# Performance work log

Hardware: AMD Instinct MI355X
Metric: run time of the kernel (lower is better)

Reference implementation:

```python
import jax, jax.numpy as jnp
import numpy as np

D_MODEL = 1024
N_HEADS = 16
SEQ_LEN = 2048
BATCH = 2
NEG = -1.0e9


def sinusoidal_embeddings(seq_len, d_k):
    # Faithful to the torch version: row 0 is all zeros; even cols get sin,
    # odd cols get cos of position/theta (theta uses the SAME index j, not j//2).
    theta = 10000.0 ** (2.0 * jnp.arange(d_k, dtype=jnp.float32) / d_k)  # [d_k]
    pos = jnp.arange(1, seq_len, dtype=jnp.float32)[:, None] / theta      # [S-1, d_k]
    even = (jnp.arange(d_k) % 2 == 0)
    body = jnp.where(even, jnp.sin(pos), jnp.cos(pos))                    # [S-1, d_k]
    return jnp.concatenate([jnp.zeros((1, d_k), dtype=pos.dtype), body], axis=0)


def setup_inputs() -> dict:
    key = jax.random.key(0)
    k_x, k_q, k_k, k_v, k_o = jax.random.split(key, 5)
    scale = 0.02
    return {
        "X": jax.random.normal(k_x, (BATCH, SEQ_LEN, D_MODEL), dtype=jnp.float32),
        "W_q": jax.random.normal(k_q, (D_MODEL, D_MODEL), dtype=jnp.float32) * scale,
        "W_k": jax.random.normal(k_k, (D_MODEL, D_MODEL), dtype=jnp.float32) * scale,
        "W_v": jax.random.normal(k_v, (D_MODEL, D_MODEL), dtype=jnp.float32) * scale,
        "W_o": jax.random.normal(k_o, (D_MODEL, D_MODEL), dtype=jnp.float32) * scale,
    }


def reference(X, W_q, W_k, W_v, W_o):
    B, S, D = X.shape
    H, d_k = N_HEADS, D // N_HEADS

    def proj(W):  # nn.Linear (no bias): y = x @ W.T, then split heads -> [B,H,S,d_k]
        return (X @ W.T).reshape(B, S, H, d_k).transpose(0, 2, 1, 3)

    Q, K, V = proj(W_q), proj(W_k), proj(W_v)

    pos = sinusoidal_embeddings(S, d_k)          # [S, d_k]
    Q = Q + pos
    K = K + pos

    mask = jnp.triu(jnp.full((S, S), NEG, dtype=X.dtype), k=1)  # [S,S]
    scores = jnp.einsum("bhqd,bhkd->bhqk", Q, K) / jnp.sqrt(jnp.float32(d_k)) + mask
    weights = jax.nn.softmax(scores, axis=-1)
    attn = jnp.einsum("bhqk,bhkd->bhqd", weights, V)            # [B,H,S,d_k]

    attn = attn.transpose(0, 2, 1, 3).reshape(B, S, D)
    return attn @ W_o.T + X
```

## Files before the change

### kernel.cpp

```cpp
#include <hip/hip_runtime.h>
#include <hip/hip_bf16.h>
#include <math.h>

#define S_LEN 2048
#define DMODEL 1024
#define NHEADS 16
#define DHEAD 64
#define NBATCH 2
#define MROWS (NBATCH * S_LEN)

typedef float f32x4 __attribute__((ext_vector_type(4)));
typedef unsigned short u16x8 __attribute__((ext_vector_type(8)));
typedef __bf16 bf16x8 __attribute__((ext_vector_type(8)));

__device__ __forceinline__ f32x4 mfma16(u16x8 a, u16x8 b, f32x4 c) {
    return __builtin_amdgcn_mfma_f32_16x16x32_bf16(
        __builtin_bit_cast(bf16x8, a), __builtin_bit_cast(bf16x8, b), c, 0, 0, 0);
}

__device__ __forceinline__ unsigned short f2bf(float f) {
    unsigned int u = __builtin_bit_cast(unsigned int, f);
    u += 0x7FFFu + ((u >> 16) & 1u);
    return (unsigned short)(u >> 16);
}

__device__ __forceinline__ unsigned int cvtpk(float lo, float hi) {
    unsigned int r;
    asm("v_cvt_pk_bf16_f32 %0, %1, %2" : "=v"(r) : "v"(lo), "v"(hi));
    return r;
}

__device__ __forceinline__ void gl16(const void* g, void* l) {
    __builtin_amdgcn_global_load_lds(
        (const __attribute__((address_space(1))) unsigned int*)g,
        (__attribute__((address_space(3))) unsigned int*)l, 16, 0, 0);
}

#define VMB(N) do { \
    asm volatile("s_waitcnt vmcnt(" #N ")" ::: "memory"); \
    __builtin_amdgcn_sched_barrier(0); \
    __builtin_amdgcn_s_barrier(); \
    __builtin_amdgcn_sched_barrier(0); } while (0)
#define PIPE_BAR_12() do { \
    asm volatile("s_waitcnt vmcnt(12)" ::: "memory"); \
    __builtin_amdgcn_sched_barrier(0); \
    __builtin_amdgcn_s_barrier(); \
    __builtin_amdgcn_sched_barrier(0); } while (0)
#define PIPE_BAR_0() do { \
    asm volatile("s_waitcnt vmcnt(0)" ::: "memory"); \
    __builtin_amdgcn_sched_barrier(0); \
    __builtin_amdgcn_s_barrier(); \
    __builtin_amdgcn_sched_barrier(0); } while (0)

__global__ __launch_bounds__(256) void cvt5(
    const float* __restrict__ X, const float* __restrict__ Wq,
    const float* __restrict__ Wk, const float* __restrict__ Wv,
    const float* __restrict__ Wo,
    unsigned short* __restrict__ Xbf, unsigned short* __restrict__ Wbf,
    float* __restrict__ pos)
{
    int b = blockIdx.x;
    if (b >= 4096) {
        int i = (b - 4096) * 256 + threadIdx.x;
        int s = i >> 6, d = i & 63;
        float theta = powf(10000.0f, (2.0f * (float)d) / 64.0f);
        float x = (float)s / theta;
        float v = (d & 1) ? cosf(x) : sinf(x);
        pos[i] = (s == 0) ? 0.0f : v;
        return;
    }
    const float* s; unsigned short* d; int t;
    if (b < 2048) { s = X; d = Xbf; t = b * 256 + threadIdx.x; }
    else {
        int z = (b - 2048) >> 9, bb = (b - 2048) & 511;
        s = (z == 0) ? Wq : (z == 1) ? Wk : (z == 2) ? Wv : Wo;
        d = Wbf + (z << 20);
        t = bb * 256 + threadIdx.x;
    }
    float4 a = *((const float4*)s + t * 2);
    float4 c = *((const float4*)s + t * 2 + 1);
    u16x8 o;
    o[0] = f2bf(a.x); o[1] = f2bf(a.y); o[2] = f2bf(a.z); o[3] = f2bf(a.w);
    o[4] = f2bf(c.x); o[5] = f2bf(c.y); o[6] = f2bf(c.z); o[7] = f2bf(c.w);
    *((u16x8*)d + t) = o;
}

__global__ __launch_bounds__(512) void gemm_qkv(
    const unsigned short* __restrict__ Xbf, const unsigned short* __restrict__ Wbf,
    const float* __restrict__ pos,
    unsigned short* __restrict__ qb, unsigned short* __restrict__ kb,
    unsigned short* __restrict__ vt)
{
    __shared__ unsigned short L[2][28672];
    const int t = threadIdx.x;
    const int lane = t & 63;
    const int w = t >> 6;
    const int wm = w >> 2, wn = w & 3;
    const int m0 = blockIdx.x * 256;
    const int nb = blockIdx.y * 192;
    const int ll = lane & 15, lg = lane >> 4;
    const int tr = t >> 3;
    const int ch = (t & 7) ^ (tr & 7);

    f32x4 acc[8][3] = {};

    const unsigned short* gA[4];
    const unsigned short* gB[3];
    #pragma unroll
    for (int i = 0; i < 4; i++)
        gA[i] = Xbf + (m0 + i * 64 + tr) * 1024 + ch * 8;
    #pragma unroll
    for (int i = 0; i < 3; i++)
        gB[i] = Wbf + (nb + i * 64 + tr) * 1024 + ch * 8;

    const int sw0 = ((0 * 4 + lg) ^ (ll & 7)) * 16;
    const int sw1 = ((1 * 4 + lg) ^ (ll & 7)) * 16;
    const int aBase = (wm * 128 + ll) * 128;
    const int bBase = 32768 + (wn * 48 + ll) * 128;
    const int wdst = w * 8 * 64;

    auto stB01 = [&](unsigned short* Ln) {
        gl16(gB[0], Ln + 16384 + wdst);          gB[0] += 64;
        gl16(gB[1], Ln + 16384 + 4096 + wdst);   gB[1] += 64;
    };
    auto stB2 = [&](unsigned short* Ln) {
        gl16(gB[2], Ln + 16384 + 8192 + wdst);   gB[2] += 64;
    };
    auto stA02 = [&](unsigned short* Ln) {
        gl16(gA[0], Ln + wdst);                  gA[0] += 64;
        gl16(gA[2], Ln + 8192 + wdst);           gA[2] += 64;
    };
    auto stA13 = [&](unsigned short* Ln) {
        gl16(gA[1], Ln + 4096 + wdst);           gA[1] += 64;
        gl16(gA[3], Ln + 12288 + wdst);          gA[3] += 64;
    };

    u16x8 bf[3][2];
    auto loadB = [&](const char* bB) {
        #pragma unroll
        for (int nf = 0; nf < 3; nf++) {
            const char* p = bB + bBase + nf * 2048;
            bf[nf][0] = *(const u16x8*)(p + sw0);
            bf[nf][1] = *(const u16x8*)(p + sw1);
        }
    };
    auto quad = [&](int q, const char* bA) {
        const char* pa = bA + aBase + q * 4096;
        u16x8 a00 = *(const u16x8*)(pa + sw0);
        u16x8 a01 = *(const u16x8*)(pa + sw1);
        u16x8 a10 = *(const u16x8*)(pa + 2048 + sw0);
        u16x8 a11 = *(const u16x8*)(pa + 2048 + sw1);
        __builtin_amdgcn_s_setprio(1);
        #pragma unroll
        for (int nf = 0; nf < 3; nf++) {
            acc[q * 2 + 0][nf] = mfma16(a00, bf[nf][0], acc[q * 2 + 0][nf]);
            acc[q * 2 + 1][nf] = mfma16(a10, bf[nf][0], acc[q * 2 + 1][nf]);
        }
        #pragma unroll
        for (int nf = 0; nf < 3; nf++) {
            acc[q * 2 + 0][nf] = mfma16(a01, bf[nf][1], acc[q * 2 + 0][nf]);
            acc[q * 2 + 1][nf] = mfma16(a11, bf[nf][1], acc[q * 2 + 1][nf]);
        }
        __builtin_amdgcn_s_setprio(0);
    };

    stB01(L[0]); stB2(L[0]); stA02(L[0]); stA13(L[0]);
    VMB(2);

    #pragma unroll 1
    for (int tt = 0; tt < 15; tt++) {
        const char* bA = (const char*)L[tt & 1];
        unsigned short* Ln = L[(tt + 1) & 1];
        stB01(Ln);
        loadB(bA);
        quad(0, bA);
        __builtin_amdgcn_s_barrier();
        stB2(Ln);
        quad(1, bA);
        __builtin_amdgcn_s_barrier();
        stA02(Ln);
        VMB(5);
        quad(2, bA);
        __builtin_amdgcn_s_barrier();
        stA13(Ln);
        quad(3, bA);
        VMB(2);
    }
    {
        const char* bA = (const char*)L[1];
        loadB(bA);
        quad(0, bA);
        __builtin_amdgcn_s_barrier();
        quad(1, bA);
        VMB(0);
        quad(2, bA);
        quad(3, bA);
    }

    #pragma unroll
    for (int nf = 0; nf < 3; nf++) {
        const int c = nb + wn * 48 + nf * 16 + ll;
        const int zz = c >> 10;
        const int lc = c & 1023;
        const int h = lc >> 6, d = lc & 63;
        if (zz == 2) {
            #pragma unroll
            for (int mf = 0; mf < 8; mf++) {
                const int row0 = m0 + wm * 128 + mf * 16 + lg * 4;
                const int b = row0 >> 11, s0 = row0 & 2047;
                unsigned long long pk =
                    (unsigned long long)cvtpk(acc[mf][nf][0], acc[mf][nf][1]) |
                    ((unsigned long long)cvtpk(acc[mf][nf][2], acc[mf][nf][3]) << 32);
                *(unsigned long long*)&vt[(((b * NHEADS + h) * 64) + d) * S_LEN + s0] = pk;
            }
        } else {
            unsigned short* const dst = (zz == 0) ? qb : kb;
            const float pscale = (zz == 0) ? 0.1803368801111244f : 1.0f;
            #pragma unroll
            for (int mf = 0; mf < 8; mf++) {
                #pragma unroll
                for (int r = 0; r < 4; r++) {
                    const int row = m0 + wm * 128 + mf * 16 + lg * 4 + r;
                    const int b = row >> 11, s = row & 2047;
                    float v = acc[mf][nf][r] + pos[s * 64 + d];
                    v *= pscale;
                    dst[(((b * NHEADS + h) * S_LEN) + s) * 64 + d] = f2bf(v);
                }
            }
        }
    }
}

__global__ __launch_bounds__(512, 4) void attn_kernel(
    const unsigned short* __restrict__ qb,
    const unsigned short* __restrict__ kb,
    const unsigned short* __restrict__ vt,
    unsigned short* __restrict__ attnb)
{
    __shared__ unsigned short Klds[2][128 * 64];
    __shared__ unsigned short Vlds[2][64 * 128];
    __shared__ unsigned short Plds[8][16 * 64];

    const int bh = blockIdx.y;
    const int x = blockIdx.x;
    const int qt = (bh < 16) ? (15 - x) : x;

    const int lane = threadIdx.x & 63;
    const int w = threadIdx.x >> 6;
    const int lg = lane >> 4, ll = lane & 15;
    const int r8 = lane >> 3, ch = (lane & 7) ^ r8;
    const int r4 = lane >> 4, c16 = lane & 15;

    const unsigned short* Q = qb + bh * (S_LEN * 64);
    const unsigned short* K = kb + bh * (S_LEN * 64);
    const unsigned short* V = vt + bh * (64 * S_LEN);
    const int q0 = qt * 128 + w * 16;

    u16x8 qf0 = *(const u16x8*)(Q + (q0 + ll) * 64 + lg * 8);
    u16x8 qf1 = *(const u16x8*)(Q + (q0 + ll) * 64 + 32 + lg * 8);

    u16x8 ones;
    #pragma unroll
    for (int i = 0; i < 8; i++) ones[i] = 0x3F80;

    f32x4 o_acc[4] = {};
    f32x4 l_acc = {};

    const int sw0 = ((0 * 4 + lg) ^ (ll & 7)) * 16;
    const int sw1 = ((1 * 4 + lg) ^ (ll & 7)) * 16;
    const char* kb0p0 = (const char*)&Klds[0][0] + ll * 128 + sw0;
    const char* kb0p1 = (const char*)&Klds[0][0] + ll * 128 + sw1;
    const char* kb1p0 = (const char*)&Klds[1][0] + ll * 128 + sw0;
    const char* kb1p1 = (const char*)&Klds[1][0] + ll * 128 + sw1;
    const char* vb0p0 = (const char*)&Vlds[0][0] + ll * 256 + sw0;
    const char* vb0p1 = (const char*)&Vlds[0][0] + ll * 256 + sw1;
    const char* vb1p0 = (const char*)&Vlds[1][0] + ll * 256 + sw0;
    const char* vb1p1 = (const char*)&Vlds[1][0] + ll * 256 + sw1;
    const int E = (ll & 7) << 4;
    char* pwb = (char*)&Plds[w][0] + (((ll * 128) + lg * 8) ^ (E & 16));
    const int pw_o0 = 0 ^ (E & 96), pw_o1 = 32 ^ (E & 96);
    const int pw_o2 = 64 ^ (E & 96), pw_o3 = 96 ^ (E & 96);
    const char* pr0 = (const char*)&Plds[w][0] + ll * 128 + sw0;
    const char* pr1 = (const char*)&Plds[w][0] + ll * 128 + sw1;
    unsigned short* kd0 = &Klds[0][(w * 16) * 64];
    unsigned short* kd1 = &Klds[1][(w * 16) * 64];
    unsigned short* vd0 = &Vlds[0][(w * 8) * 128];
    unsigned short* vd1 = &Vlds[1][(w * 8) * 128];
    const unsigned short* gk  = K + (w * 16 + r8) * 64 + ch * 8;
    const unsigned short* gva = V + (w * 8 + r4) * S_LEN + ((c16 ^ r4) * 8);
    const unsigned short* gvb = V + (w * 8 + 4 + r4) * S_LEN + ((c16 ^ (4 + r4)) * 8);
    const int dthr = w * 16 + ll - lg * 4;

    auto stage2 = [&](unsigned short* kd, unsigned short* vd) {
        gl16(gk, kd);
        gl16(gk + 512, kd + 512);
        gl16(gva, vd);
        gl16(gvb, vd + 512);
        gk += 128 * 64;
        gva += 128;
        gvb += 128;
    };

    auto tile_body = [&](const char* kp0, const char* kp1,
                         const char* vp0, const char* vp1, bool masked, int thr) {
        f32x4 sc[4] = {};
        __builtin_amdgcn_s_setprio(1);
        #pragma unroll
        for (int f = 0; f < 4; f++) {
            const u16x8 kfa = *(const u16x8*)(kp0 + f * 2048);
            sc[f] = mfma16(kfa, qf0, sc[f]);
            const u16x8 kfb = *(const u16x8*)(kp1 + f * 2048);
            sc[f] = mfma16(kfb, qf1, sc[f]);
        }
        __builtin_amdgcn_s_setprio(0);
        if (masked) {
            #pragma unroll
            for (int f = 0; f < 4; f++)
                #pragma unroll
                for (int r = 0; r < 4; r++)
                    if (f * 16 + r > thr) sc[f][r] = -1.0e9f;
        }
        #pragma unroll
        for (int f = 0; f < 4; f++)
            #pragma unroll
            for (int r = 0; r < 4; r++)
                sc[f][r] = __builtin_amdgcn_exp2f(sc[f][r]);
        *(unsigned long long*)(pwb + pw_o0) =
            (unsigned long long)cvtpk(sc[0][0], sc[0][1]) | ((unsigned long long)cvtpk(sc[0][2], sc[0][3]) << 32);
        *(unsigned long long*)(pwb + pw_o1) =
            (unsigned long long)cvtpk(sc[1][0], sc[1][1]) | ((unsigned long long)cvtpk(sc[1][2], sc[1][3]) << 32);
        *(unsigned long long*)(pwb + pw_o2) =
            (unsigned long long)cvtpk(sc[2][0], sc[2][1]) | ((unsigned long long)cvtpk(sc[2][2], sc[2][3]) << 32);
        *(unsigned long long*)(pwb + pw_o3) =
            (unsigned long long)cvtpk(sc[3][0], sc[3][1]) | ((unsigned long long)cvtpk(sc[3][2], sc[3][3]) << 32);
        const u16x8 pf0 = *(const u16x8*)pr0;
        const u16x8 pf1 = *(const u16x8*)pr1;
        __builtin_amdgcn_s_setprio(1);
        #pragma unroll
        for (int f = 0; f < 4; f++) {
            o_acc[f] = mfma16(pf0, *(const u16x8*)(vp0 + f * 4096), o_acc[f]);
            o_acc[f] = mfma16(pf1, *(const u16x8*)(vp1 + f * 4096), o_acc[f]);
        }
        l_acc = mfma16(pf0, ones, l_acc);
        l_acc = mfma16(pf1, ones, l_acc);
        __builtin_amdgcn_s_setprio(0);
    };

    auto body128_full = [&](const char* kp0, const char* kp1,
                            const char* vp0, const char* vp1) {
        tile_body(kp0, kp1, vp0, vp1, false, 0);
        tile_body(kp0 + 8192, kp1 + 8192, vp0 + 128, vp1 + 128, false, 0);
    };
    auto body128_diag = [&](const char* kp0, const char* kp1,
                            const char* vp0, const char* vp1) {
        tile_body(kp0, kp1, vp0, vp1, true, dthr);
        if (w >= 4)
            tile_body(kp0 + 8192, kp1 + 8192, vp0 + 128, vp1 + 128, true, dthr - 64);
    };

    stage2(kd0, vd0);
    __syncthreads();

    int p = 0;
    while (p + 2 <= qt) {
        stage2(kd1, vd1);
        body128_full(kb0p0, kb0p1, vb0p0, vb0p1);
        __syncthreads();
        stage2(kd0, vd0);
        body128_full(kb1p0, kb1p1, vb1p0, vb1p1);
        __syncthreads();
        p += 2;
    }
    if (p < qt) {
        stage2(kd1, vd1);
        body128_full(kb0p0, kb0p1, vb0p0, vb0p1);
        __syncthreads();
        body128_diag(kb1p0, kb1p1, vb1p0, vb1p1);
    } else {
        body128_diag(kb0p0, kb0p1, vb0p0, vb0p1);
    }

    const int bb = bh >> 4, h = bh & 15;
    const float lr0 = 1.0f / l_acc[0];
    const float lr1 = 1.0f / l_acc[1];
    const float lr2 = 1.0f / l_acc[2];
    const float lr3 = 1.0f / l_acc[3];
    #pragma unroll
    for (int f = 0; f < 4; f++) {
        const int colbase = h * 64 + f * 16 + ll;
        attnb[(bb * S_LEN + q0 + lg * 4 + 0) * DMODEL + colbase] = f2bf(o_acc[f][0] * lr0);
        attnb[(bb * S_LEN + q0 + lg * 4 + 1) * DMODEL + colbase] = f2bf(o_acc[f][1] * lr1);
        attnb[(bb * S_LEN + q0 + lg * 4 + 2) * DMODEL + colbase] = f2bf(o_acc[f][2] * lr2);
        attnb[(bb * S_LEN + q0 + lg * 4 + 3) * DMODEL + colbase] = f2bf(o_acc[f][3] * lr3);
    }
}

__global__ __launch_bounds__(128) void gemm_out(
    const unsigned short* __restrict__ Abf,
    const unsigned short* __restrict__ Wbf,
    const float* __restrict__ X,
    float* __restrict__ out)
{
    const unsigned short* __restrict__ W = Wbf + (3u << 20);
    __shared__ unsigned short L[3][192 * 64];
    const int t = threadIdx.x;
    const int lane = t & 63;
    const int w = t >> 6;
    const int m0 = blockIdx.x * 128;
    const int n0 = blockIdx.y * 64;
    const int ll = lane & 15, lg = lane >> 4;
    const int r8 = lane >> 3, ch = (lane & 7) ^ r8;

    f32x4 acc[4][4] = {};

    const unsigned short* gA[8];
    const unsigned short* gB[4];
    #pragma unroll
    for (int i = 0; i < 8; i++) gA[i] = Abf + (m0 + w * 64 + i * 8 + r8) * 1024 + ch * 8;
    #pragma unroll
    for (int i = 0; i < 4; i++) gB[i] = W + (n0 + w * 32 + i * 8 + r8) * 1024 + ch * 8;

    const int sw0 = ((0 * 4 + lg) ^ (ll & 7)) * 16;
    const int sw1 = ((1 * 4 + lg) ^ (ll & 7)) * 16;

    auto stage = [&](unsigned short* Lb) {
        unsigned short* const dA = Lb + (w * 64) * 64;
        unsigned short* const dB = Lb + 128 * 64 + (w * 32) * 64;
        #pragma unroll
        for (int i = 0; i < 8; i++) { gl16(gA[i], dA + i * 8 * 64); gA[i] += 64; }
        #pragma unroll
        for (int i = 0; i < 4; i++) { gl16(gB[i], dB + i * 8 * 64); gB[i] += 64; }
    };
    auto compute = [&](const unsigned short* Lb) {
        const char* const pA0 = (const char*)Lb + (w * 64 + ll) * 128 + sw0;
        const char* const pA1 = (const char*)Lb + (w * 64 + ll) * 128 + sw1;
        const char* const pB0 = (const char*)Lb + 16384 + ll * 128 + sw0;
        const char* const pB1 = (const char*)Lb + 16384 + ll * 128 + sw1;
        u16x8 af[4], bfv[4];
        #pragma unroll
        for (int m = 0; m < 4; m++) af[m] = *(const u16x8*)(pA0 + m * 2048);
        #pragma unroll
        for (int n = 0; n < 4; n++) bfv[n] = *(const u16x8*)(pB0 + n * 2048);
        __builtin_amdgcn_s_setprio(1);
        #pragma unroll
        for (int m = 0; m < 4; m++)
            #pragma unroll
            for (int n = 0; n < 4; n++)
                acc[m][n] = mfma16(af[m], bfv[n], acc[m][n]);
        __builtin_amdgcn_s_setprio(0);
        #pragma unroll
        for (int m = 0; m < 4; m++) af[m] = *(const u16x8*)(pA1 + m * 2048);
        #pragma unroll
        for (int n = 0; n < 4; n++) bfv[n] = *(const u16x8*)(pB1 + n * 2048);
        __builtin_amdgcn_s_setprio(1);
        #pragma unroll
        for (int m = 0; m < 4; m++)
            #pragma unroll
            for (int n = 0; n < 4; n++)
                acc[m][n] = mfma16(af[m], bfv[n], acc[m][n]);
        __builtin_amdgcn_s_setprio(0);
    };

    stage(L[0]);
    stage(L[1]);
    PIPE_BAR_12();
    for (int tt = 0; tt < 4; tt++) {
        stage(L[2]); compute(L[0]); PIPE_BAR_12();
        stage(L[0]); compute(L[1]); PIPE_BAR_12();
        stage(L[1]); compute(L[2]); PIPE_BAR_12();
    }
    stage(L[2]); compute(L[0]); PIPE_BAR_12();
    stage(L[0]); compute(L[1]); PIPE_BAR_12();
    compute(L[2]); PIPE_BAR_0();
    compute(L[0]);

    #pragma unroll
    for (int m = 0; m < 4; m++)
        #pragma unroll
        for (int n = 0; n < 4; n++)
            #pragma unroll
            for (int r = 0; r < 4; r++) {
                const int row = m0 + w * 64 + m * 16 + lg * 4 + r;
                const int col = n0 + n * 16 + ll;
                out[row * 1024 + col] = acc[m][n][r] + X[row * 1024 + col];
            }
}

extern "C" void kernel_launch(void* const* d_in, const int* in_sizes, int n_in,
                              void* d_out, int out_size, void* d_ws, size_t ws_size,
                              hipStream_t stream) {
    const float* X  = (const float*)d_in[0];
    const float* Wq = (const float*)d_in[1];
    const float* Wk = (const float*)d_in[2];
    const float* Wv = (const float*)d_in[3];
    const float* Wo = (const float*)d_in[4];
    float* out = (float*)d_out;

    char* ws = (char*)d_ws;
    float*          pos  = (float*)(ws);
    unsigned short* Xbf  = (unsigned short*)(ws + (512u << 10));
    unsigned short* Wbf  = (unsigned short*)(ws + (512u << 10) + (8u  << 20));
    unsigned short* qb   = (unsigned short*)(ws + (512u << 10) + (16u << 20));
    unsigned short* kb   = (unsigned short*)(ws + (512u << 10) + (24u << 20));
    unsigned short* vt   = (unsigned short*)(ws + (512u << 10) + (32u << 20));
    unsigned short* attb = Xbf;

    cvt5<<<dim3(4608), dim3(256), 0, stream>>>(X, Wq, Wk, Wv, Wo, Xbf, Wbf, pos);
    gemm_qkv<<<dim3(16, 16), dim3(512), 0, stream>>>(Xbf, Wbf, pos, qb, kb, vt);
    attn_kernel<<<dim3(16, 32), dim3(512), 0, stream>>>(qb, kb, vt, attb);
    gemm_out<<<dim3(32, 16), dim3(128), 0, stream>>>(attb, Wbf, X, out);
}
```

Baseline: 90.59 us.

## Restructure output GEMM to 128x128 tiles with 8 waves and interleaved staging

```diff
diff --git a/kernel.cpp b/kernel.cpp
--- a/kernel.cpp
+++ b/kernel.cpp
@@ -38,16 +38,6 @@
 
 #define VMB(N) do { \
     asm volatile("s_waitcnt vmcnt(" #N ")" ::: "memory"); \
-    __builtin_amdgcn_sched_barrier(0); \
-    __builtin_amdgcn_s_barrier(); \
-    __builtin_amdgcn_sched_barrier(0); } while (0)
-#define PIPE_BAR_12() do { \
-    asm volatile("s_waitcnt vmcnt(12)" ::: "memory"); \
-    __builtin_amdgcn_sched_barrier(0); \
-    __builtin_amdgcn_s_barrier(); \
-    __builtin_amdgcn_sched_barrier(0); } while (0)
-#define PIPE_BAR_0() do { \
-    asm volatile("s_waitcnt vmcnt(0)" ::: "memory"); \
     __builtin_amdgcn_sched_barrier(0); \
     __builtin_amdgcn_s_barrier(); \
     __builtin_amdgcn_sched_barrier(0); } while (0)
@@ -241,8 +231,8 @@
     __shared__ unsigned short Vlds[2][64 * 128];
     __shared__ unsigned short Plds[8][16 * 64];
 
-    const int bh = blockIdx.y;
-    const int x = blockIdx.x;
+    const int bh = blockIdx.x;
+    const int x = blockIdx.y;
     const int qt = (bh < 16) ? (15 - x) : x;
 
     const int lane = threadIdx.x & 63;
@@ -395,94 +385,106 @@
     }
 }
 
-__global__ __launch_bounds__(128) void gemm_out(
+__global__ __launch_bounds__(512) void gemm_out(
     const unsigned short* __restrict__ Abf,
     const unsigned short* __restrict__ Wbf,
     const float* __restrict__ X,
     float* __restrict__ out)
 {
     const unsigned short* __restrict__ W = Wbf + (3u << 20);
-    __shared__ unsigned short L[3][192 * 64];
+    __shared__ unsigned short L[3][16384];
     const int t = threadIdx.x;
     const int lane = t & 63;
     const int w = t >> 6;
+    const int wm = w >> 2, wn = w & 3;
     const int m0 = blockIdx.x * 128;
-    const int n0 = blockIdx.y * 64;
+    const int n0 = blockIdx.y * 128;
     const int ll = lane & 15, lg = lane >> 4;
-    const int r8 = lane >> 3, ch = (lane & 7) ^ r8;
-
-    f32x4 acc[4][4] = {};
-
-    const unsigned short* gA[8];
-    const unsigned short* gB[4];
-    #pragma unroll
-    for (int i = 0; i < 8; i++) gA[i] = Abf + (m0 + w * 64 + i * 8 + r8) * 1024 + ch * 8;
-    #pragma unroll
-    for (int i = 0; i < 4; i++) gB[i] = W + (n0 + w * 32 + i * 8 + r8) * 1024 + ch * 8;
+    const int tr = t >> 3;
+    const int ch = (t & 7) ^ (tr & 7);
+
+    f32x4 acc[4][2] = {};
+
+    const unsigned short* gA[2];
+    const unsigned short* gB[2];
+    #pragma unroll
+    for (int i = 0; i < 2; i++) {
+        gA[i] = Abf + (m0 + i * 64 + tr) * 1024 + ch * 8;
+        gB[i] = W + (n0 + i * 64 + tr) * 1024 + ch * 8;
+    }
 
     const int sw0 = ((0 * 4 + lg) ^ (ll & 7)) * 16;
     const int sw1 = ((1 * 4 + lg) ^ (ll & 7)) * 16;
-
-    auto stage = [&](unsigned short* Lb) {
-        unsigned short* const dA = Lb + (w * 64) * 64;
-        unsigned short* const dB = Lb + 128 * 64 + (w * 32) * 64;
-        #pragma unroll
-        for (int i = 0; i < 8; i++) { gl16(gA[i], dA + i * 8 * 64); gA[i] += 64; }
-        #pragma unroll
-        for (int i = 0; i < 4; i++) { gl16(gB[i], dB + i * 8 * 64); gB[i] += 64; }
-    };
-    auto compute = [&](const unsigned short* Lb) {
-        const char* const pA0 = (const char*)Lb + (w * 64 + ll) * 128 + sw0;
-        const char* const pA1 = (const char*)Lb + (w * 64 + ll) * 128 + sw1;
-        const char* const pB0 = (const char*)Lb + 16384 + ll * 128 + sw0;
-        const char* const pB1 = (const char*)Lb + 16384 + ll * 128 + sw1;
-        u16x8 af[4], bfv[4];
-        #pragma unroll
-        for (int m = 0; m < 4; m++) af[m] = *(const u16x8*)(pA0 + m * 2048);
-        #pragma unroll
-        for (int n = 0; n < 4; n++) bfv[n] = *(const u16x8*)(pB0 + n * 2048);
+    const int aBase = (wm * 64 + ll) * 128;
+    const int bBase = 16384 + (wn * 32 + ll) * 128;
+    const int wdst = w * 8 * 64;
+
+    auto stA0 = [&](unsigned short* Ln) { gl16(gA[0], Ln + wdst);        gA[0] += 64; };
+    auto stA1 = [&](unsigned short* Ln) { gl16(gA[1], Ln + 4096 + wdst); gA[1] += 64; };
+    auto stB0 = [&](unsigned short* Ln) { gl16(gB[0], Ln + 8192 + wdst); gB[0] += 64; };
+    auto stB1 = [&](unsigned short* Ln) { gl16(gB[1], Ln + 12288 + wdst); gB[1] += 64; };
+
+    u16x8 bfv[2][2];
+    auto loadB = [&](const char* bb) {
+        #pragma unroll
+        for (int nf = 0; nf < 2; nf++) {
+            const char* p = bb + bBase + nf * 2048;
+            bfv[nf][0] = *(const u16x8*)(p + sw0);
+            bfv[nf][1] = *(const u16x8*)(p + sw1);
+        }
+    };
+    auto quad = [&](int mf, const char* bb) {
+        const char* pa = bb + aBase + mf * 2048;
+        u16x8 a0 = *(const u16x8*)(pa + sw0);
+        u16x8 a1 = *(const u16x8*)(pa + sw1);
         __builtin_amdgcn_s_setprio(1);
         #pragma unroll
-        for (int m = 0; m < 4; m++)
-            #pragma unroll
-            for (int n = 0; n < 4; n++)
-                acc[m][n] = mfma16(af[m], bfv[n], acc[m][n]);
+        for (int nf = 0; nf < 2; nf++)
+            acc[mf][nf] = mfma16(a0, bfv[nf][0], acc[mf][nf]);
+        #pragma unroll
+        for (int nf = 0; nf < 2; nf++)
+            acc[mf][nf] = mfma16(a1, bfv[nf][1], acc[mf][nf]);
         __builtin_amdgcn_s_setprio(0);
-        #pragma unroll
-        for (int m = 0; m < 4; m++) af[m] = *(const u16x8*)(pA1 + m * 2048);
-        #pragma unroll
-        for (int n = 0; n < 4; n++) bfv[n] = *(const u16x8*)(pB1 + n * 2048);
-        __builtin_amdgcn_s_setprio(1);
-        #pragma unroll
-        for (int m = 0; m < 4; m++)
-            #pragma unroll
-            for (int n = 0; n < 4; n++)
-                acc[m][n] = mfma16(af[m], bfv[n], acc[m][n]);
-        __builtin_amdgcn_s_setprio(0);
-    };
-
-    stage(L[0]);
-    stage(L[1]);
-    PIPE_BAR_12();
+    };
+
+    auto ktile = [&](const char* bb, unsigned short* Ln, bool stg) {
+        if (stg) stA0(Ln);
+        loadB(bb);
+        quad(0, bb);
+        __builtin_amdgcn_s_barrier();
+        if (stg) stA1(Ln);
+        quad(1, bb);
+        __builtin_amdgcn_s_barrier();
+        if (stg) stB0(Ln);
+        quad(2, bb);
+        __builtin_amdgcn_s_barrier();
+        if (stg) stB1(Ln);
+        quad(3, bb);
+    };
+
+    stA0(L[0]); stA1(L[0]); stB0(L[0]); stB1(L[0]);
+    stA0(L[1]); stA1(L[1]); stB0(L[1]); stB1(L[1]);
+    VMB(4);
+    #pragma unroll 1
     for (int tt = 0; tt < 4; tt++) {
-        stage(L[2]); compute(L[0]); PIPE_BAR_12();
-        stage(L[0]); compute(L[1]); PIPE_BAR_12();
-        stage(L[1]); compute(L[2]); PIPE_BAR_12();
-    }
-    stage(L[2]); compute(L[0]); PIPE_BAR_12();
-    stage(L[0]); compute(L[1]); PIPE_BAR_12();
-    compute(L[2]); PIPE_BAR_0();
-    compute(L[0]);
-
-    #pragma unroll
-    for (int m = 0; m < 4; m++)
-        #pragma unroll
-        for (int n = 0; n < 4; n++)
+        ktile((const char*)L[0], L[2], true); VMB(4);
+        ktile((const char*)L[1], L[0], true); VMB(4);
+        ktile((const char*)L[2], L[1], true); VMB(4);
+    }
+    ktile((const char*)L[0], L[2], true); VMB(4);
+    ktile((const char*)L[1], L[0], true); VMB(4);
+    ktile((const char*)L[2], nullptr, false); VMB(0);
+    ktile((const char*)L[0], nullptr, false);
+
+    #pragma unroll
+    for (int mf = 0; mf < 4; mf++)
+        #pragma unroll
+        for (int nf = 0; nf < 2; nf++)
             #pragma unroll
             for (int r = 0; r < 4; r++) {
-                const int row = m0 + w * 64 + m * 16 + lg * 4 + r;
-                const int col = n0 + n * 16 + ll;
-                out[row * 1024 + col] = acc[m][n][r] + X[row * 1024 + col];
+                const int row = m0 + wm * 64 + mf * 16 + lg * 4 + r;
+                const int col = n0 + wn * 32 + nf * 16 + ll;
+                out[row * 1024 + col] = acc[mf][nf][r] + X[row * 1024 + col];
             }
 }
 
@@ -507,6 +509,6 @@
 
     cvt5<<<dim3(4608), dim3(256), 0, stream>>>(X, Wq, Wk, Wv, Wo, Xbf, Wbf, pos);
     gemm_qkv<<<dim3(16, 16), dim3(512), 0, stream>>>(Xbf, Wbf, pos, qb, kb, vt);
-    attn_kernel<<<dim3(16, 32), dim3(512), 0, stream>>>(qb, kb, vt, attb);
-    gemm_out<<<dim3(32, 16), dim3(128), 0, stream>>>(attb, Wbf, X, out);
-}
+    attn_kernel<<<dim3(32, 16), dim3(512), 0, stream>>>(qb, kb, vt, attb);
+    gemm_out<<<dim3(32, 8), dim3(512), 0, stream>>>(attb, Wbf, X, out);
+}
```

New measurement: 94.96 us. 4.8% more time.
